# Optimization experiments

Measured on AMD Instinct MI355X. Metric: run time of the kernel, lower is better.

## Reference

```python
import jax, jax.numpy as jnp
import numpy as np

SOFTCAP = 30.0  # final_logit_softcapping (Gemma2)


def setup_inputs() -> dict:
    key = jax.random.key(0)
    ks = jax.random.split(key, 6)
    B, S, D, V = 32, 8, 2048, 128000
    return {
        "embedding": jax.random.normal(ks[0], (V, D), jnp.float32) * 0.02,
        "hidden_states": jax.random.normal(ks[1], (B, S, D), jnp.float32),
        "temperatures": jax.random.uniform(ks[2], (B,), jnp.float32, 0.5, 1.0),
        "top_ps": jax.random.uniform(ks[3], (B,), jnp.float32, 0.5, 1.0),
        "output_positions": jax.random.randint(ks[4], (1,), 0, S),
        "top_ks": jax.random.randint(ks[5], (B,), 1, 64),
    }


def reference(embedding, hidden_states, temperatures, top_ps, output_positions, top_ks):
    # select decode position: [B, 1, D] -> [B, D]
    hs = jnp.take(hidden_states, output_positions, axis=1).squeeze(1)
    # logits over vocab: [B, V]
    logits = jnp.einsum("bd,vd->bv", hs, embedding)
    # final logit softcapping
    logits = jnp.tanh(logits / SOFTCAP) * SOFTCAP
    # temperature scaling (matches in-place div; returned logits are scaled)
    logits = logits / temperatures[:, None]
    probs = jax.nn.softmax(logits.astype(jnp.float32), axis=-1)
    # sort descending
    idx = jnp.argsort(-probs, axis=-1)                      # [B, V]
    probs_sort = jnp.take_along_axis(probs, idx, axis=-1)   # [B, V]
    cum = jnp.cumsum(probs_sort, axis=-1)
    V = probs.shape[-1]
    mask = ((cum - probs_sort) > top_ps[:, None]) | (
        jnp.arange(V)[None, :] >= top_ks[:, None]
    )
    probs_sort = jnp.where(mask, 0.0, probs_sort)
    probs_sort = probs_sort / probs_sort.sum(axis=-1, keepdims=True)
    # scatter back to vocab order
    inv = jnp.argsort(idx, axis=-1)
    probs_final = jnp.take_along_axis(probs_sort, inv, axis=-1)
    # multinomial sample (one draw per row)
    next_token_ids = jax.random.categorical(
        jax.random.key(42), jnp.log(probs_final), axis=-1
    )
    return next_token_ids, logits
```

## Files before the change

### kernel.cpp

```cpp
#include <hip/hip_runtime.h>
#include <float.h>
#include <math.h>

#define VOCAB 128000
#define DIM   2048
#define SEQL  8
#define NB    32
#define SCAP  4096

__device__ __forceinline__ unsigned f2sortable(float x){
  unsigned u = __float_as_uint(x);
  return (u & 0x80000000u) ? ~u : (u | 0x80000000u);
}
__device__ __forceinline__ unsigned rotl32(unsigned x, int d){
  return (x << d) | (x >> (32 - d));
}

__device__ float jax_gumbel(unsigned n){
  unsigned x0 = 0u, x1 = n;
  const unsigned k0 = 0u, k1 = 42u;
  const unsigned k2 = 0x1BD11BDAu ^ k0 ^ k1;
  x0 += k0; x1 += k1;
#define TFR(r) { x0 += x1; x1 = rotl32(x1, r); x1 ^= x0; }
  TFR(13) TFR(15) TFR(26) TFR(6)
  x0 += k1; x1 += k2 + 1u;
  TFR(17) TFR(29) TFR(16) TFR(24)
  x0 += k2; x1 += k0 + 2u;
  TFR(13) TFR(15) TFR(26) TFR(6)
  x0 += k0; x1 += k1 + 3u;
  TFR(17) TFR(29) TFR(16) TFR(24)
  x0 += k1; x1 += k2 + 4u;
  TFR(13) TFR(15) TFR(26) TFR(6)
  x0 += k2; x1 += k0 + 5u;
#undef TFR
  unsigned bits = x0 ^ x1;
  float f = __uint_as_float((bits >> 9) | 0x3f800000u) - 1.0f;
  float u = f + 1.17549435e-38f;
  return -logf(-logf(u));
}

__global__ __launch_bounds__(256, 4) void k_logits(
    const float* __restrict__ E, const float* __restrict__ HS,
    const float* __restrict__ temps, const int* __restrict__ posp,
    float* __restrict__ C)
{
  __shared__ float hs_s[2][NB * 64];
  __shared__ float tile[NB * 32];
  const int tid  = threadIdx.x;
  const int w    = tid >> 6;
  const int lane = tid & 63;
  const int g    = lane >> 4;
  const int qi   = lane & 15;
  const int pos  = posp[0];
  const int vbase = blockIdx.x * 32;
  const int vw    = vbase + w * 8;
  const int bofs  = blockIdx.x & 31;

  float acc[8][8];
#pragma unroll
  for (int j = 0; j < 8; ++j)
#pragma unroll
    for (int bl = 0; bl < 8; ++bl) acc[j][bl] = 0.f;

  const int sb0 = w * 8 + g;
  const int sb1 = w * 8 + 4 + g;
  const float* hsp0 = HS + ((size_t)(sb0 * SEQL + pos)) * DIM + qi * 4;
  const float* hsp1 = HS + ((size_t)(sb1 * SEQL + pos)) * DIM + qi * 4;
  const int lo0 = sb0 * 64 + qi * 4;
  const int lo1 = sb1 * 64 + qi * 4;

  {
    float4 a = *(const float4*)(hsp0 + bofs * 64);
    float4 c = *(const float4*)(hsp1 + bofs * 64);
    *(float4*)&hs_s[0][lo0] = a;
    *(float4*)&hs_s[0][lo1] = c;
  }

  const float* Eb = E + (size_t)vw * DIM + qi * 4;

  for (int si = 0; si < 32; ++si){
    const int s = (si + bofs) & 31;
    __syncthreads();
    float4 e[8];
#pragma unroll
    for (int j = 0; j < 8; ++j)
      e[j] = *(const float4*)(Eb + (size_t)j * DIM + s * 64);
    float4 n0, n1;
    const bool more = (si + 1 < 32);
    const int sn = (si + 1 + bofs) & 31;
    if (more){
      n0 = *(const float4*)(hsp0 + sn * 64);
      n1 = *(const float4*)(hsp1 + sn * 64);
    }
    const float* hb = &hs_s[si & 1][0];
#pragma unroll
    for (int bl = 0; bl < 8; ++bl){
      float4 h = *(const float4*)(hb + (g * 8 + bl) * 64 + qi * 4);
#pragma unroll
      for (int j = 0; j < 8; ++j){
        acc[j][bl] = fmaf(e[j].x, h.x, acc[j][bl]);
        acc[j][bl] = fmaf(e[j].y, h.y, acc[j][bl]);
        acc[j][bl] = fmaf(e[j].z, h.z, acc[j][bl]);
        acc[j][bl] = fmaf(e[j].w, h.w, acc[j][bl]);
      }
    }
    if (more){
      float* wb = &hs_s[(si + 1) & 1][0];
      *(float4*)&wb[lo0] = n0;
      *(float4*)&wb[lo1] = n1;
    }
  }

#pragma unroll
  for (int j = 0; j < 8; ++j)
#pragma unroll
    for (int bl = 0; bl < 8; ++bl){
      float v = acc[j][bl];
      v += __shfl_xor(v, 1, 64);
      v += __shfl_xor(v, 2, 64);
      v += __shfl_xor(v, 4, 64);
      v += __shfl_xor(v, 8, 64);
      acc[j][bl] = v;
    }
  if (qi == 0){
#pragma unroll
    for (int j = 0; j < 8; ++j)
#pragma unroll
      for (int bl = 0; bl < 8; ++bl)
        tile[(g * 8 + bl) * 32 + w * 8 + j] = acc[j][bl];
  }
  __syncthreads();
  {
    const int b = tid >> 3, vq = tid & 7;
    const float tmp = temps[b];
    float4 tv = *(const float4*)&tile[b * 32 + vq * 4];
    float4 o;
    o.x = (tanhf(tv.x / 30.f) * 30.f) / tmp;
    o.y = (tanhf(tv.y / 30.f) * 30.f) / tmp;
    o.z = (tanhf(tv.z / 30.f) * 30.f) / tmp;
    o.w = (tanhf(tv.w / 30.f) * 30.f) / tmp;
    *(float4*)(C + (size_t)b * VOCAB + vbase + vq * 4) = o;
  }
}

__global__ __launch_bounds__(1024) void k_sample_fused(
    const float* __restrict__ C,
    const float* __restrict__ tps, const int* __restrict__ tks,
    float* __restrict__ out_tok)
{
  const int b = blockIdx.x, t = threadIdx.x;
  const float* row = C + (size_t)b * VOCAB;
  __shared__ float redm[1024];
  __shared__ float reds[1024];
  __shared__ unsigned ps[1024];
  __shared__ unsigned hist[4096];
  __shared__ float    cval_s[SCAP];
  __shared__ int      cidx_s[SCAP];
  __shared__ int tbin_s;
  __shared__ unsigned cnt_s;

  if (t == 0) cnt_s = 0u;
  for (int i = t; i < 4096; i += 1024) hist[i] = 0u;
  __syncthreads();

  float m_run = -FLT_MAX, zs = 0.f;
  for (int f = t; f < VOCAB / 4; f += 1024){
    float4 x4 = ((const float4*)row)[f];
    float xs[4] = {x4.x, x4.y, x4.z, x4.w};
    float mx = fmaxf(fmaxf(xs[0], xs[1]), fmaxf(xs[2], xs[3]));
    float nm = fmaxf(m_run, mx);
    zs = zs * expf(m_run - nm);
#pragma unroll
    for (int c = 0; c < 4; ++c){
      zs += expf(xs[c] - nm);
      atomicAdd(&hist[f2sortable(xs[c]) >> 20], 1u);
    }
    m_run = nm;
  }
  redm[t] = m_run; reds[t] = zs; __syncthreads();
  for (int sft = 512; sft > 0; sft >>= 1){
    if (t < sft){
      float m1 = redm[t], s1 = reds[t];
      float m2 = redm[t + sft], s2 = reds[t + sft];
      float nm = fmaxf(m1, m2);
      redm[t] = nm;
      reds[t] = s1 * expf(m1 - nm) + s2 * expf(m2 - nm);
    }
    __syncthreads();
  }
  const float m = redm[0], Z = reds[0];

  unsigned s_t = 0u;
#pragma unroll
  for (int k = 0; k < 4; ++k) s_t += hist[t * 4 + k];
  ps[t] = s_t; __syncthreads();
  for (int off = 1; off < 1024; off <<= 1){
    unsigned v = ps[t] + ((t + off < 1024) ? ps[t + off] : 0u);
    __syncthreads();
    ps[t] = v;
    __syncthreads();
  }
  const unsigned Sstrict = ps[t] - s_t;
  if (Sstrict < 64u && ps[t] >= 64u){
    unsigned c = Sstrict;
    for (int bb = 3; bb >= 0; --bb){
      c += hist[t * 4 + bb];
      if (c >= 64u){ tbin_s = t * 4 + bb; break; }
    }
  }
  __syncthreads();
  const unsigned thr = ((unsigned)tbin_s) << 20;

  for (int f = t; f < VOCAB / 4; f += 1024){
    float4 x4 = ((const float4*)row)[f];
    float xs[4] = {x4.x, x4.y, x4.z, x4.w};
#pragma unroll
    for (int c = 0; c < 4; ++c){
      if (f2sortable(xs[c]) >= thr){
        unsigned slot = atomicAdd(&cnt_s, 1u);
        if (slot < (unsigned)SCAP){
          cval_s[slot] = xs[c];
          cidx_s[slot] = f * 4 + c;
        }
      }
    }
  }
  __syncthreads();
  int cn = (int)cnt_s; if (cn > SCAP) cn = SCAP;

  for (int j = t; j < cn; j += 1024)
    cval_s[j] = expf(cval_s[j] - m) / Z;
  __syncthreads();

  if (t < 64){
    float my_sp = 0.f; int my_si = 0;
    float lp = FLT_MAX; int li = -1;
    for (int r = 0; r < 64; ++r){
      float bp = -1.f; int bi = 0x7fffffff;
      for (int j = t; j < cn; j += 64){
        float p = cval_s[j]; int id = cidx_s[j];
        bool valid = (p < lp) || (p == lp && id > li);
        if (valid && (p > bp || (p == bp && id < bi))){ bp = p; bi = id; }
      }
#pragma unroll
      for (int off = 32; off >= 1; off >>= 1){
        float op = __shfl_xor(bp, off, 64);
        int   oi = __shfl_xor(bi, off, 64);
        if (op > bp || (op == bp && oi < bi)){ bp = op; bi = oi; }
      }
      if (t == r){ my_sp = bp; my_si = bi; }
      lp = bp; li = bi;
    }

    const float tp = tps[b];
    const int   tk = tks[b];
    float c = 0.f, sren = 0.f;
    bool keep_me = false;
    for (int j = 0; j < 64; ++j){
      float pj = __shfl(my_sp, j, 64);
      c = c + pj;
      float excl = c - pj;
      bool keep = (!(excl > tp)) && (j < tk);
      if (j == t) keep_me = keep;
      if (keep) sren = sren + pj;
    }

    float score = -FLT_MAX;
    int vid = my_si;
    if (keep_me){
      float pf = my_sp / sren;
      score = logf(pf) + jax_gumbel((unsigned)(b * VOCAB + vid));
    }
    float bs = score; int bv = vid;
#pragma unroll
    for (int off = 32; off >= 1; off >>= 1){
      float os = __shfl_xor(bs, off, 64);
      int   ov = __shfl_xor(bv, off, 64);
      if (os > bs || (os == bs && ov < bv)){ bs = os; bv = ov; }
    }
    if (t == 0) out_tok[b] = (float)bv;
  }
}

extern "C" void kernel_launch(void* const* d_in, const int* in_sizes, int n_in,
                              void* d_out, int out_size, void* d_ws, size_t ws_size,
                              hipStream_t stream)
{
  (void)in_sizes; (void)n_in; (void)out_size; (void)d_ws; (void)ws_size;
  const float* emb   = (const float*)d_in[0];
  const float* hs    = (const float*)d_in[1];
  const float* temps = (const float*)d_in[2];
  const float* tps   = (const float*)d_in[3];
  const int*   posp  = (const int*)d_in[4];
  const int*   tks   = (const int*)d_in[5];
  float* out = (float*)d_out;
  float* C   = out + NB;

  k_logits      <<<dim3(VOCAB / 32), dim3(256),  0, stream>>>(emb, hs, temps, posp, C);
  k_sample_fused<<<dim3(NB),         dim3(1024), 0, stream>>>(C, tps, tks, out);
}
```

Baseline: 421.0 us.

## Split per-row sampling kernel into segmented multi-block stats, threshold, collect, sample

Replaces the single 32-block sampling kernel, one block per row, with four kernels. Two of them spread each vocab row over 8 blocks (256 blocks in total) to compute the partial max/sum-exp and histogram and then collect candidates. The partial results are merged through global workspace with atomics plus a small threshold kernel. The aim is to use more compute units than the 32 the old kernel occupied on the memory-bound scans. The cost is extra launches, a memset, global atomics and a round trip through global memory for the candidates.

New measurement: 425.2 us. Within noise of the previous version (+1.0%).

```diff
diff --git a/kernel.cpp b/kernel.cpp
--- a/kernel.cpp
+++ b/kernel.cpp
@@ -7,6 +7,8 @@
 #define SEQL  8
 #define NB    32
 #define SCAP  4096
+#define NSEG  8
+#define F4SEG 4000
 
 __device__ __forceinline__ unsigned f2sortable(float x){
   unsigned u = __float_as_uint(x);
@@ -143,28 +145,21 @@
   }
 }
 
-__global__ __launch_bounds__(1024) void k_sample_fused(
-    const float* __restrict__ C,
-    const float* __restrict__ tps, const int* __restrict__ tks,
-    float* __restrict__ out_tok)
-{
-  const int b = blockIdx.x, t = threadIdx.x;
+__global__ __launch_bounds__(1024) void k_stats_part(
+    const float* __restrict__ C, unsigned* __restrict__ hist_g,
+    float* __restrict__ pm, float* __restrict__ pz)
+{
+  const int bid = blockIdx.x, b = bid >> 3, seg = bid & 7;
+  const int t = threadIdx.x;
   const float* row = C + (size_t)b * VOCAB;
-  __shared__ float redm[1024];
-  __shared__ float reds[1024];
-  __shared__ unsigned ps[1024];
   __shared__ unsigned hist[4096];
-  __shared__ float    cval_s[SCAP];
-  __shared__ int      cidx_s[SCAP];
-  __shared__ int tbin_s;
-  __shared__ unsigned cnt_s;
-
-  if (t == 0) cnt_s = 0u;
+  __shared__ float redm[1024], reds[1024];
   for (int i = t; i < 4096; i += 1024) hist[i] = 0u;
   __syncthreads();
 
+  const int f0 = seg * F4SEG, f1 = f0 + F4SEG;
   float m_run = -FLT_MAX, zs = 0.f;
-  for (int f = t; f < VOCAB / 4; f += 1024){
+  for (int f = f0 + t; f < f1; f += 1024){
     float4 x4 = ((const float4*)row)[f];
     float xs[4] = {x4.x, x4.y, x4.z, x4.w};
     float mx = fmaxf(fmaxf(xs[0], xs[1]), fmaxf(xs[2], xs[3]));
@@ -188,11 +183,35 @@
     }
     __syncthreads();
   }
-  const float m = redm[0], Z = reds[0];
+  if (t == 0){ pm[b * 8 + seg] = redm[0]; pz[b * 8 + seg] = reds[0]; }
+  __syncthreads();
+  for (int i = t; i < 4096; i += 1024)
+    if (hist[i]) atomicAdd(&hist_g[b * 4096 + i], hist[i]);
+}
+
+__global__ __launch_bounds__(1024) void k_thresh(
+    const unsigned* __restrict__ hist_g, const float* __restrict__ pm,
+    const float* __restrict__ pz, unsigned* __restrict__ thr_g,
+    float* __restrict__ mz_g)
+{
+  const int b = blockIdx.x, t = threadIdx.x;
+  __shared__ unsigned hl[4096];
+  __shared__ unsigned ps[1024];
+  __shared__ int tbin_s;
+
+  float m = pm[b * 8];
+#pragma unroll
+  for (int s2 = 1; s2 < 8; ++s2) m = fmaxf(m, pm[b * 8 + s2]);
+  float Z = 0.f;
+#pragma unroll
+  for (int s2 = 0; s2 < 8; ++s2) Z += pz[b * 8 + s2] * expf(pm[b * 8 + s2] - m);
+
+  for (int i = t; i < 4096; i += 1024) hl[i] = hist_g[b * 4096 + i];
+  __syncthreads();
 
   unsigned s_t = 0u;
 #pragma unroll
-  for (int k = 0; k < 4; ++k) s_t += hist[t * 4 + k];
+  for (int k = 0; k < 4; ++k) s_t += hl[t * 4 + k];
   ps[t] = s_t; __syncthreads();
   for (int off = 1; off < 1024; off <<= 1){
     unsigned v = ps[t] + ((t + off < 1024) ? ps[t + off] : 0u);
@@ -204,32 +223,60 @@
   if (Sstrict < 64u && ps[t] >= 64u){
     unsigned c = Sstrict;
     for (int bb = 3; bb >= 0; --bb){
-      c += hist[t * 4 + bb];
+      c += hl[t * 4 + bb];
       if (c >= 64u){ tbin_s = t * 4 + bb; break; }
     }
   }
   __syncthreads();
-  const unsigned thr = ((unsigned)tbin_s) << 20;
-
-  for (int f = t; f < VOCAB / 4; f += 1024){
+  if (t == 0){
+    thr_g[b] = ((unsigned)tbin_s) << 20;
+    mz_g[b * 2] = m; mz_g[b * 2 + 1] = Z;
+  }
+}
+
+__global__ __launch_bounds__(1024) void k_collect(
+    const float* __restrict__ C, const unsigned* __restrict__ thr_g,
+    unsigned* __restrict__ cnt_g, float* __restrict__ cval_g,
+    int* __restrict__ cidx_g)
+{
+  const int bid = blockIdx.x, b = bid >> 3, seg = bid & 7;
+  const int t = threadIdx.x;
+  const unsigned thr = thr_g[b];
+  const float* row = C + (size_t)b * VOCAB;
+  const int f0 = seg * F4SEG, f1 = f0 + F4SEG;
+  for (int f = f0 + t; f < f1; f += 1024){
     float4 x4 = ((const float4*)row)[f];
     float xs[4] = {x4.x, x4.y, x4.z, x4.w};
 #pragma unroll
     for (int c = 0; c < 4; ++c){
       if (f2sortable(xs[c]) >= thr){
-        unsigned slot = atomicAdd(&cnt_s, 1u);
+        unsigned slot = atomicAdd(&cnt_g[b], 1u);
         if (slot < (unsigned)SCAP){
-          cval_s[slot] = xs[c];
-          cidx_s[slot] = f * 4 + c;
+          cval_g[b * SCAP + slot] = xs[c];
+          cidx_g[b * SCAP + slot] = f * 4 + c;
         }
       }
     }
   }
-  __syncthreads();
-  int cn = (int)cnt_s; if (cn > SCAP) cn = SCAP;
-
-  for (int j = t; j < cn; j += 1024)
-    cval_s[j] = expf(cval_s[j] - m) / Z;
+}
+
+__global__ __launch_bounds__(1024) void k_sample(
+    const float* __restrict__ tps, const int* __restrict__ tks,
+    const unsigned* __restrict__ cnt_g, const float* __restrict__ cval_g,
+    const int* __restrict__ cidx_g, const float* __restrict__ mz_g,
+    float* __restrict__ out_tok)
+{
+  const int b = blockIdx.x, t = threadIdx.x;
+  __shared__ float cval_s[SCAP];
+  __shared__ int   cidx_s[SCAP];
+  const float m = mz_g[b * 2], Z = mz_g[b * 2 + 1];
+  unsigned cnu = cnt_g[b];
+  int cn = (cnu > (unsigned)SCAP) ? SCAP : (int)cnu;
+
+  for (int j = t; j < cn; j += 1024){
+    cval_s[j] = expf(cval_g[b * SCAP + j] - m) / Z;
+    cidx_s[j] = cidx_g[b * SCAP + j];
+  }
   __syncthreads();
 
   if (t < 64){
@@ -286,7 +333,7 @@
                               void* d_out, int out_size, void* d_ws, size_t ws_size,
                               hipStream_t stream)
 {
-  (void)in_sizes; (void)n_in; (void)out_size; (void)d_ws; (void)ws_size;
+  (void)in_sizes; (void)n_in; (void)out_size; (void)ws_size;
   const float* emb   = (const float*)d_in[0];
   const float* hs    = (const float*)d_in[1];
   const float* temps = (const float*)d_in[2];
@@ -296,6 +343,20 @@
   float* out = (float*)d_out;
   float* C   = out + NB;
 
-  k_logits      <<<dim3(VOCAB / 32), dim3(256),  0, stream>>>(emb, hs, temps, posp, C);
-  k_sample_fused<<<dim3(NB),         dim3(1024), 0, stream>>>(C, tps, tks, out);
-}
+  unsigned* hist_g = (unsigned*)d_ws;
+  unsigned* cnt_g  = hist_g + 32 * 4096;
+  float*    pm     = (float*)(cnt_g + 32);
+  float*    pz     = pm + 256;
+  unsigned* thr_g  = (unsigned*)(pz + 256);
+  float*    mz_g   = (float*)(thr_g + 32);
+  float*    cval_g = mz_g + 64;
+  int*      cidx_g = (int*)(cval_g + 32 * SCAP);
+
+  hipMemsetAsync(d_ws, 0, (size_t)(32 * 4096 + 32) * 4, stream);
+
+  k_logits    <<<dim3(VOCAB / 32), dim3(256),  0, stream>>>(emb, hs, temps, posp, C);
+  k_stats_part<<<dim3(NB * NSEG),  dim3(1024), 0, stream>>>(C, hist_g, pm, pz);
+  k_thresh    <<<dim3(NB),         dim3(1024), 0, stream>>>(hist_g, pm, pz, thr_g, mz_g);
+  k_collect   <<<dim3(NB * NSEG),  dim3(1024), 0, stream>>>(C, thr_g, cnt_g, cval_g, cidx_g);
+  k_sample    <<<dim3(NB),         dim3(1024), 0, stream>>>(tps, tks, cnt_g, cval_g, cidx_g, mz_g, out);
+}
```

## Build per-row logit histograms in the logits kernel to drop a sampling pass

Applied to the files above, without the earlier changes.

The logits kernel now adds each output value into a per-row global 4096-bin histogram using global atomics, after the workspace is zeroed with a memset. The sampling kernel loads that histogram, finds the top-64 threshold bin first, and then gathers candidates during the same pass that computes max and sum-exp. This removes one full read of each 128000-element logits row and the shared-memory histogram atomics. In exchange it adds global atomic contention, since 4000 blocks hit the same 32 histograms, plus a memset launch.

Result: slower. 490.9 us (+16.6%).

```diff
diff --git a/kernel.cpp b/kernel.cpp
--- a/kernel.cpp
+++ b/kernel.cpp
@@ -42,7 +42,7 @@
 __global__ __launch_bounds__(256, 4) void k_logits(
     const float* __restrict__ E, const float* __restrict__ HS,
     const float* __restrict__ temps, const int* __restrict__ posp,
-    float* __restrict__ C)
+    float* __restrict__ C, unsigned* __restrict__ hist_g)
 {
   __shared__ float hs_s[2][NB * 64];
   __shared__ float tile[NB * 32];
@@ -140,28 +140,54 @@
     o.z = (tanhf(tv.z / 30.f) * 30.f) / tmp;
     o.w = (tanhf(tv.w / 30.f) * 30.f) / tmp;
     *(float4*)(C + (size_t)b * VOCAB + vbase + vq * 4) = o;
+    unsigned* hb_ = hist_g + b * 4096;
+    atomicAdd(&hb_[f2sortable(o.x) >> 20], 1u);
+    atomicAdd(&hb_[f2sortable(o.y) >> 20], 1u);
+    atomicAdd(&hb_[f2sortable(o.z) >> 20], 1u);
+    atomicAdd(&hb_[f2sortable(o.w) >> 20], 1u);
   }
 }
 
 __global__ __launch_bounds__(1024) void k_sample_fused(
     const float* __restrict__ C,
     const float* __restrict__ tps, const int* __restrict__ tks,
-    float* __restrict__ out_tok)
+    const unsigned* __restrict__ hist_g, float* __restrict__ out_tok)
 {
   const int b = blockIdx.x, t = threadIdx.x;
   const float* row = C + (size_t)b * VOCAB;
+  __shared__ unsigned hl[4096];
+  __shared__ unsigned ps[1024];
   __shared__ float redm[1024];
   __shared__ float reds[1024];
-  __shared__ unsigned ps[1024];
-  __shared__ unsigned hist[4096];
   __shared__ float    cval_s[SCAP];
   __shared__ int      cidx_s[SCAP];
   __shared__ int tbin_s;
   __shared__ unsigned cnt_s;
 
   if (t == 0) cnt_s = 0u;
-  for (int i = t; i < 4096; i += 1024) hist[i] = 0u;
-  __syncthreads();
+  for (int i = t; i < 4096; i += 1024) hl[i] = hist_g[b * 4096 + i];
+  __syncthreads();
+
+  unsigned s_t = 0u;
+#pragma unroll
+  for (int k = 0; k < 4; ++k) s_t += hl[t * 4 + k];
+  ps[t] = s_t; __syncthreads();
+  for (int off = 1; off < 1024; off <<= 1){
+    unsigned v = ps[t] + ((t + off < 1024) ? ps[t + off] : 0u);
+    __syncthreads();
+    ps[t] = v;
+    __syncthreads();
+  }
+  const unsigned Sstrict = ps[t] - s_t;
+  if (Sstrict < 64u && ps[t] >= 64u){
+    unsigned c = Sstrict;
+    for (int bb = 3; bb >= 0; --bb){
+      c += hl[t * 4 + bb];
+      if (c >= 64u){ tbin_s = t * 4 + bb; break; }
+    }
+  }
+  __syncthreads();
+  const unsigned thr = ((unsigned)tbin_s) << 20;
 
   float m_run = -FLT_MAX, zs = 0.f;
   for (int f = t; f < VOCAB / 4; f += 1024){
@@ -173,7 +199,13 @@
 #pragma unroll
     for (int c = 0; c < 4; ++c){
       zs += expf(xs[c] - nm);
-      atomicAdd(&hist[f2sortable(xs[c]) >> 20], 1u);
+      if (f2sortable(xs[c]) >= thr){
+        unsigned slot = atomicAdd(&cnt_s, 1u);
+        if (slot < (unsigned)SCAP){
+          cval_s[slot] = xs[c];
+          cidx_s[slot] = f * 4 + c;
+        }
+      }
     }
     m_run = nm;
   }
@@ -189,43 +221,6 @@
     __syncthreads();
   }
   const float m = redm[0], Z = reds[0];
-
-  unsigned s_t = 0u;
-#pragma unroll
-  for (int k = 0; k < 4; ++k) s_t += hist[t * 4 + k];
-  ps[t] = s_t; __syncthreads();
-  for (int off = 1; off < 1024; off <<= 1){
-    unsigned v = ps[t] + ((t + off < 1024) ? ps[t + off] : 0u);
-    __syncthreads();
-    ps[t] = v;
-    __syncthreads();
-  }
-  const unsigned Sstrict = ps[t] - s_t;
-  if (Sstrict < 64u && ps[t] >= 64u){
-    unsigned c = Sstrict;
-    for (int bb = 3; bb >= 0; --bb){
-      c += hist[t * 4 + bb];
-      if (c >= 64u){ tbin_s = t * 4 + bb; break; }
-    }
-  }
-  __syncthreads();
-  const unsigned thr = ((unsigned)tbin_s) << 20;
-
-  for (int f = t; f < VOCAB / 4; f += 1024){
-    float4 x4 = ((const float4*)row)[f];
-    float xs[4] = {x4.x, x4.y, x4.z, x4.w};
-#pragma unroll
-    for (int c = 0; c < 4; ++c){
-      if (f2sortable(xs[c]) >= thr){
-        unsigned slot = atomicAdd(&cnt_s, 1u);
-        if (slot < (unsigned)SCAP){
-          cval_s[slot] = xs[c];
-          cidx_s[slot] = f * 4 + c;
-        }
-      }
-    }
-  }
-  __syncthreads();
   int cn = (int)cnt_s; if (cn > SCAP) cn = SCAP;
 
   for (int j = t; j < cn; j += 1024)
@@ -286,7 +281,7 @@
                               void* d_out, int out_size, void* d_ws, size_t ws_size,
                               hipStream_t stream)
 {
-  (void)in_sizes; (void)n_in; (void)out_size; (void)d_ws; (void)ws_size;
+  (void)in_sizes; (void)n_in; (void)out_size; (void)ws_size;
   const float* emb   = (const float*)d_in[0];
   const float* hs    = (const float*)d_in[1];
   const float* temps = (const float*)d_in[2];
@@ -296,6 +291,9 @@
   float* out = (float*)d_out;
   float* C   = out + NB;
 
-  k_logits      <<<dim3(VOCAB / 32), dim3(256),  0, stream>>>(emb, hs, temps, posp, C);
-  k_sample_fused<<<dim3(NB),         dim3(1024), 0, stream>>>(C, tps, tks, out);
-}
+  unsigned* hist_g = (unsigned*)d_ws;
+  hipMemsetAsync(hist_g, 0, (size_t)NB * 4096 * sizeof(unsigned), stream);
+
+  k_logits      <<<dim3(VOCAB / 32), dim3(256),  0, stream>>>(emb, hs, temps, posp, C, hist_g);
+  k_sample_fused<<<dim3(NB),         dim3(1024), 0, stream>>>(C, tps, tks, hist_g, out);
+}
```
